# Kernel tuning notes

Measured on AMD Instinct MI355X. Metric: run time of the kernel, lower is better.

## Reference

```python
import jax, jax.numpy as jnp
import numpy as np

B, T, H, V = 32, 256, 1024, 50257


def setup_inputs() -> dict:
    key = jax.random.key(0)
    k1, k2, k3, k4 = jax.random.split(key, 4)
    # log-normalized HMM parameters, matching torch.log_softmax in __init__
    alpha = jax.nn.log_softmax(jax.random.normal(k1, (H, H), dtype=jnp.float32), axis=1)
    beta = jax.nn.log_softmax(jax.random.normal(k2, (H, V), dtype=jnp.float32), axis=1)
    gamma = jax.nn.log_softmax(jax.random.normal(k3, (H,), dtype=jnp.float32), axis=0)
    x = jax.random.randint(k4, (B, T), 0, V)
    return {"x": x, "alpha": alpha, "beta": beta, "gamma": gamma}


def reference(x, alpha, beta, gamma):
    # emission log-probs gathered per token: e[b, t, h] = beta[h, x[b, t]]
    e = beta.T[x]  # [B, T, H]

    # backward-in-time recurrence:
    #   y_{T-1} = e[:, T-1]
    #   y_t     = logsumexp_j(alpha[i, j] + y_{t+1}[b, j]) + e[:, t]
    y0 = e[:, -1]  # [B, H]

    def step(y, e_t):
        y = jax.nn.logsumexp(alpha[None, :, :] + y[:, None, :], axis=2) + e_t
        return y, None

    # scan over t = T-2 .. 0 (reverse time order)
    es = jnp.flip(e[:, :-1], axis=1).transpose(1, 0, 2)  # [T-1, B, H]
    y, _ = jax.lax.scan(step, y0, es)

    # final marginalization over initial-state distribution gamma
    return jax.nn.logsumexp(gamma[None, :] + y, axis=1)  # [B]
```

## Files before the change

kernel.cpp:

```cpp
#include <hip/hip_runtime.h>
#include <hip/hip_bf16.h>


#define Hdim 1024
#define Bdim 32
#define Tdim 256
#define Vdim 50257
#define NWG  16
#define SLICE 64

typedef __attribute__((ext_vector_type(8))) __bf16 bf16x8;
typedef __attribute__((ext_vector_type(4))) float  f32x4;
typedef __attribute__((ext_vector_type(4))) unsigned u32x4;

#define OFF_ABF   0
#define OFF_YBUF  2097152
#define OFF_PSUM  (OFF_YBUF + 131072)
#define OFF_RBUF  (OFF_PSUM + 128)
#define OFF_LREC  (OFF_RBUF + 128)
#define OFF_END0  (OFF_LREC + 8192)
#define OFF_E     (((OFF_END0) + 4095) & ~4095)
#define WS_E_NEED ((size_t)OFF_E + (size_t)Tdim * Bdim * Hdim * 4)

#define SM_A       131072
#define SM_YSH     (SM_A)
#define SM_GSH     (SM_YSH + 4096)
#define SM_LTILE   (SM_GSH + 128)
#define SMEM_BYTES (SM_LTILE + 512)

__device__ __forceinline__ void st_b128_sc(void* p, u32x4 v) {
    asm volatile("global_store_dwordx4 %0, %1, off sc0 sc1" :: "v"(p), "v"(v) : "memory");
}
__device__ __forceinline__ void st_b32_sc(void* p, unsigned v) {
    asm volatile("global_store_dword %0, %1, off sc0 sc1" :: "v"(p), "v"(v) : "memory");
}
__device__ __forceinline__ void st_f32_sc(void* p, float v) {
    asm volatile("global_store_dword %0, %1, off sc0 sc1" :: "v"(p), "v"(v) : "memory");
}
__device__ __forceinline__ u32x4 ld_b128_sc(const void* p) {
    u32x4 r;
    asm volatile("global_load_dwordx4 %0, %1, off sc0 sc1" : "=v"(r) : "v"(p) : "memory");
    return r;
}
__device__ __forceinline__ float ld_f32_sc(const void* p) {
    float r;
    asm volatile("global_load_dword %0, %1, off sc0 sc1" : "=v"(r) : "v"(p) : "memory");
    return r;
}
__device__ __forceinline__ void waitcnt_vm0() {
    asm volatile("s_waitcnt vmcnt(0)" ::: "memory");
    __builtin_amdgcn_sched_barrier(0);
}

__global__ void k_expA(const float* __restrict__ alpha, __bf16* __restrict__ Abf) {
    int idx = (blockIdx.x * 256 + threadIdx.x) * 4;
    float4 v = *(const float4*)(alpha + idx);
    union { __bf16 h[4]; uint2 u; } cv;
    cv.h[0] = (__bf16)__expf(v.x);
    cv.h[1] = (__bf16)__expf(v.y);
    cv.h[2] = (__bf16)__expf(v.z);
    cv.h[3] = (__bf16)__expf(v.w);
    *(uint2*)(Abf + idx) = cv.u;
}

__global__ void k_gather(const int* __restrict__ x, const float* __restrict__ beta,
                         float* __restrict__ E) {
    int tb = blockIdx.x;
    int t  = tb >> 5, b = tb & 31;
    int xv = x[b * Tdim + t];
    int i  = threadIdx.x * 4;
    float4 v;
    v.x = beta[(size_t)(i + 0) * Vdim + xv];
    v.y = beta[(size_t)(i + 1) * Vdim + xv];
    v.z = beta[(size_t)(i + 2) * Vdim + xv];
    v.w = beta[(size_t)(i + 3) * Vdim + xv];
    *(float4*)(E + ((size_t)t * Bdim + b) * Hdim + i) = v;
}

__device__ __forceinline__ void wait_flags(const char* lrec, int par, unsigned want) {
    if (threadIdx.x < 64) {
        const unsigned* fp =
            (const unsigned*)(lrec + ((size_t)par * NWG + (threadIdx.x & 15)) * 256 + 128);
        while (!__all((int)(__hip_atomic_load(fp, __ATOMIC_RELAXED, __HIP_MEMORY_SCOPE_AGENT) >= want)))
            __builtin_amdgcn_s_sleep(1);
    }
    __syncthreads();
}

__device__ __forceinline__ void load_e(const float* __restrict__ E,
                                       const float* __restrict__ beta,
                                       const int* __restrict__ x,
                                       int t, int b0, int i0, int useE, float e[2][4]) {
    if (useE) {
        #pragma unroll
        for (int u = 0; u < 2; ++u)
            #pragma unroll
            for (int r = 0; r < 4; ++r)
                e[u][r] = E[((size_t)t * Bdim + (b0 + r)) * Hdim + i0 + u * 16];
    } else {
        int xv[4];
        #pragma unroll
        for (int r = 0; r < 4; ++r) xv[r] = x[(b0 + r) * Tdim + t];
        #pragma unroll
        for (int u = 0; u < 2; ++u)
            #pragma unroll
            for (int r = 0; r < 4; ++r)
                e[u][r] = beta[(size_t)(i0 + u * 16) * Vdim + xv[r]];
    }
}

__device__ __forceinline__ void store_phase(const float y[2][4], const float Gc[4],
                                            char* Yblk,
                                            char* Lrec_p,
                                            __bf16* Ysh, float* Ltile,
                                            int w, int li, int g, int np, int b0,
                                            unsigned seq) {
    #pragma unroll
    for (int r = 0; r < 4; ++r) {
        #pragma unroll
        for (int u = 0; u < 2; ++u) {
            float Yn = __expf(y[u][r] - Gc[r]);
            Ysh[(b0 + r) * 64 + np * 32 + u * 16 + li] = (__bf16)Yn;
        }
        float m = fmaxf(y[0][r], y[1][r]);
        m = fmaxf(m, __shfl_xor(m, 1, 16));
        m = fmaxf(m, __shfl_xor(m, 2, 16));
        m = fmaxf(m, __shfl_xor(m, 4, 16));
        m = fmaxf(m, __shfl_xor(m, 8, 16));
        if (li == 0) Ltile[w * 32 + b0 + r] = m;
    }
    __syncthreads();
    const int tid = threadIdx.x;
    st_b128_sc(Yblk + tid * 16, ((const u32x4*)Ysh)[tid]);
    if (tid < 32) {
        int mbb = tid >> 4;
        float L = fmaxf(Ltile[mbb * 32 + tid], Ltile[(mbb + 2) * 32 + tid]);
        st_f32_sc(Lrec_p + tid * 4, L);
    }
    asm volatile("s_waitcnt vmcnt(0)" ::: "memory");
    __syncthreads();
    if (tid == 0) st_b32_sc(Lrec_p + 128, seq);
}

__launch_bounds__(256, 1)
__global__ void k_hmm(const int* __restrict__ x,
                      const float* __restrict__ beta,
                      const float* __restrict__ gamma,
                      const __bf16* __restrict__ Abf,
                      char* __restrict__ Yb,
                      char* __restrict__ lrec,
                      float* __restrict__ Psum,
                      float* __restrict__ Rbuf,
                      const float* __restrict__ Ebuf,
                      int useE)
{
    extern __shared__ char smem[];
    char*   Asl   = smem;
    __bf16* Ysh   = (__bf16*)(smem + SM_YSH);
    float*  Gsh   = (float*)(smem + SM_GSH);
    float*  Ltile = (float*)(smem + SM_LTILE);

    const int p   = blockIdx.x;
    const int tid = threadIdx.x;
    const int w   = tid >> 6;
    const int l   = tid & 63;
    const int g   = l >> 4;
    const int li  = l & 15;
    const int mb  = w & 1;
    const int np  = w >> 1;
    const int b0  = mb * 16 + g * 4;
    const int i0  = p * SLICE + np * 32 + li;

    #pragma unroll
    for (int rep = 0; rep < 32; ++rep) {
        int flat = rep * 256 + tid;
        int row  = flat >> 7;
        int c16  = flat & 127;
        uint4 v = *(const uint4*)((const char*)Abf + (size_t)(p * 64 + row) * 2048 + c16 * 16);
        int off = (row * 2048 + c16 * 16) ^ ((row & 7) << 4);
        *(uint4*)(Asl + off) = v;
    }
    __syncthreads();

    {
        float y0[2][4];
        load_e(Ebuf, beta, x, Tdim - 1, b0, i0, useE, y0);
        float Gc0[4] = {0.f, 0.f, 0.f, 0.f};
        store_phase(y0, Gc0, Yb + p * 4096, lrec + (size_t)p * 256,
                    Ysh, Ltile, w, li, g, np, b0, 1u);
    }

    float Nprev[4] = {0.f, 0.f, 0.f, 0.f};
    float ereg[2][4];
    load_e(Ebuf, beta, x, Tdim - 2, b0, i0, useE, ereg);

    for (int s = 1; s < Tdim; ++s) {
        const int t     = Tdim - 1 - s;
        const int par_r = (s - 1) & 1;
        const int par_w = s & 1;

        float eregN[2][4];
        if (s < Tdim - 1) load_e(Ebuf, beta, x, t - 1, b0, i0, useE, eregN);

        float gl[2] = {0.f, 0.f};
        if (s == Tdim - 1) { gl[0] = gamma[i0]; gl[1] = gamma[i0 + 16]; }

        wait_flags(lrec, par_r, (unsigned)s);

        const char* Ybase = Yb + (size_t)par_r * (NWG * 4096);
        const char* yrow  = Ybase + (mb * 16 + li) * 128 + g * 16;
        u32x4 yreg[32];
        #pragma unroll
        for (int kc = 0; kc < 32; ++kc)
            yreg[kc] = ld_b128_sc(yrow + (kc >> 1) * 4096 + (kc & 1) * 64);

        float gmv[16];
        const char* lbase = lrec + (size_t)par_r * NWG * 256;
        if (tid < 32) {
            #pragma unroll
            for (int q = 0; q < 16; ++q)
                gmv[q] = ld_f32_sc(lbase + q * 256 + tid * 4);
        }

        waitcnt_vm0();

        if (tid < 32) {
            float gm = gmv[0];
            #pragma unroll
            for (int q = 1; q < 16; ++q) gm = fmaxf(gm, gmv[q]);
            Gsh[tid] = gm;
        }
        __syncthreads();

        f32x4 acc0 = {0.f, 0.f, 0.f, 0.f}, acc1 = {0.f, 0.f, 0.f, 0.f};
        {
            const int ia = np * 32 + li;
            const int ib = ia + 16;
            const int basea = ia * 2048 + g * 16, xa = (ia & 7) << 4;
            const int baseb = ib * 2048 + g * 16, xb = (ib & 7) << 4;
            #pragma unroll
            for (int kc = 0; kc < 32; ++kc) {
                bf16x8 af0 = *(const bf16x8*)(Asl + ((basea + kc * 64) ^ xa));
                bf16x8 af1 = *(const bf16x8*)(Asl + ((baseb + kc * 64) ^ xb));
                bf16x8 yf  = __builtin_bit_cast(bf16x8, yreg[kc]);
                acc0 = __builtin_amdgcn_mfma_f32_16x16x32_bf16(yf, af0, acc0, 0, 0, 0);
                acc1 = __builtin_amdgcn_mfma_f32_16x16x32_bf16(yf, af1, acc1, 0, 0, 0);
            }
        }

        float Gcur[4];
        #pragma unroll
        for (int r = 0; r < 4; ++r) Gcur[r] = Gsh[b0 + r];

        float yv[2][4];
        #pragma unroll
        for (int r = 0; r < 4; ++r) {
            yv[0][r] = Nprev[r] + __logf(acc0[r]) + ereg[0][r];
            yv[1][r] = Nprev[r] + __logf(acc1[r]) + ereg[1][r];
        }

        if (s < Tdim - 1) {
            store_phase(yv, Gcur, Yb + (size_t)par_w * (NWG * 4096) + p * 4096,
                        lrec + ((size_t)par_w * NWG + p) * 256,
                        Ysh, Ltile, w, li, g, np, b0, (unsigned)(s + 1));
            #pragma unroll
            for (int r = 0; r < 4; ++r) Nprev[r] = Gcur[r];
            #pragma unroll
            for (int u = 0; u < 2; ++u)
                #pragma unroll
                for (int r = 0; r < 4; ++r) ereg[u][r] = eregN[u][r];
        } else {
            #pragma unroll
            for (int r = 0; r < 4; ++r) {
                float pa = __expf(gl[0] + yv[0][r] - Gcur[r])
                         + __expf(gl[1] + yv[1][r] - Gcur[r]);
                pa += __shfl_xor(pa, 1, 16);
                pa += __shfl_xor(pa, 2, 16);
                pa += __shfl_xor(pa, 4, 16);
                pa += __shfl_xor(pa, 8, 16);
                if (li == 0) {
                    atomicAdd(&Psum[b0 + r], pa);
                    if (p == 0) Rbuf[b0 + r] = Gcur[r];
                }
            }
        }
    }
}

__global__ void k_final(const float* __restrict__ Psum, const float* __restrict__ Rbuf,
                        float* __restrict__ out) {
    int b = threadIdx.x;
    if (b < 32) out[b] = Rbuf[b] + __logf(Psum[b]);
}

extern "C" void kernel_launch(void* const* d_in, const int* in_sizes, int n_in,
                              void* d_out, int out_size, void* d_ws, size_t ws_size,
                              hipStream_t stream) {
    const int*   x     = (const int*)d_in[0];
    const float* alpha = (const float*)d_in[1];
    const float* beta  = (const float*)d_in[2];
    const float* gamma = (const float*)d_in[3];

    char* ws = (char*)d_ws;
    __bf16* Abf  = (__bf16*)(ws + OFF_ABF);
    char*   Yb   = ws + OFF_YBUF;
    float*  Psum = (float*)(ws + OFF_PSUM);
    float*  Rbuf = (float*)(ws + OFF_RBUF);
    char*   lrec = ws + OFF_LREC;
    float*  Ebuf = (float*)(ws + OFF_E);

    int useE = (ws_size >= WS_E_NEED) ? 1 : 0;

    (void)hipMemsetAsync(ws + OFF_PSUM, 0, OFF_END0 - OFF_PSUM, stream);

    hipLaunchKernelGGL(k_expA, dim3((Hdim * Hdim) / (256 * 4)), dim3(256), 0, stream, alpha, Abf);

    if (useE)
        hipLaunchKernelGGL(k_gather, dim3(Tdim * Bdim), dim3(256), 0, stream, x, beta, Ebuf);

    (void)hipFuncSetAttribute((const void*)k_hmm, hipFuncAttributeMaxDynamicSharedMemorySize, SMEM_BYTES);
    hipLaunchKernelGGL(k_hmm, dim3(NWG), dim3(256), SMEM_BYTES, stream,
                       x, beta, gamma, Abf, Yb, lrec, Psum, Rbuf,
                       useE ? Ebuf : (const float*)nullptr, useE);

    hipLaunchKernelGGL(k_final, dim3(1), dim3(64), 0, stream, Psum, Rbuf, (float*)d_out);
}
```

Before: 2.119 ms.

## Co-locate persistent workgroups on one XCC and use cheaper cache-scope sync

The launch grows to 512 workgroups. The first workgroups found on one XCC (home chosen by CAS on the XCC id) claim the 16 compute slots and the rest exit. A runtime handshake then checks that plain sc0 stores and loads are visible across the 16 workgroups. If they are, the recurrence runs with sc0-only global accesses instead of sc0 sc1 system-scope ones, cutting the latency of each inter-workgroup exchange per timestep. The cost is extra launch overhead, a verification phase, and reliance on residency and cache-coherence behaviour, with a fallback to the old path if the check fails.

```diff
diff --git a/kernel.cpp b/kernel.cpp
--- a/kernel.cpp
+++ b/kernel.cpp
@@ -8,6 +8,8 @@
 #define Vdim 50257
 #define NWG  16
 #define SLICE 64
+#define NBLK 512
+#define VBOUND 1500
 
 typedef __attribute__((ext_vector_type(8))) __bf16 bf16x8;
 typedef __attribute__((ext_vector_type(4))) float  f32x4;
@@ -18,7 +20,9 @@
 #define OFF_PSUM  (OFF_YBUF + 131072)
 #define OFF_RBUF  (OFF_PSUM + 128)
 #define OFF_LREC  (OFF_RBUF + 128)
-#define OFF_END0  (OFF_LREC + 8192)
+#define OFF_CTL   (OFF_LREC + 8192)
+#define OFF_VER   (OFF_CTL + 128)
+#define OFF_END0  (OFF_VER + 256)
 #define OFF_E     (((OFF_END0) + 4095) & ~4095)
 #define WS_E_NEED ((size_t)OFF_E + (size_t)Tdim * Bdim * Hdim * 4)
 
@@ -28,23 +32,54 @@
 #define SM_LTILE   (SM_GSH + 128)
 #define SMEM_BYTES (SM_LTILE + 512)
 
-__device__ __forceinline__ void st_b128_sc(void* p, u32x4 v) {
-    asm volatile("global_store_dwordx4 %0, %1, off sc0 sc1" :: "v"(p), "v"(v) : "memory");
-}
-__device__ __forceinline__ void st_b32_sc(void* p, unsigned v) {
-    asm volatile("global_store_dword %0, %1, off sc0 sc1" :: "v"(p), "v"(v) : "memory");
-}
-__device__ __forceinline__ void st_f32_sc(void* p, float v) {
-    asm volatile("global_store_dword %0, %1, off sc0 sc1" :: "v"(p), "v"(v) : "memory");
-}
-__device__ __forceinline__ u32x4 ld_b128_sc(const void* p) {
+template<bool SC1>
+__device__ __forceinline__ void st_b128_x(void* p, u32x4 v) {
+    if constexpr (SC1)
+        asm volatile("global_store_dwordx4 %0, %1, off sc0 sc1" :: "v"(p), "v"(v) : "memory");
+    else
+        asm volatile("global_store_dwordx4 %0, %1, off sc0" :: "v"(p), "v"(v) : "memory");
+}
+template<bool SC1>
+__device__ __forceinline__ void st_b32_x(void* p, unsigned v) {
+    if constexpr (SC1)
+        asm volatile("global_store_dword %0, %1, off sc0 sc1" :: "v"(p), "v"(v) : "memory");
+    else
+        asm volatile("global_store_dword %0, %1, off sc0" :: "v"(p), "v"(v) : "memory");
+}
+template<bool SC1>
+__device__ __forceinline__ void st_f32_x(void* p, float v) {
+    if constexpr (SC1)
+        asm volatile("global_store_dword %0, %1, off sc0 sc1" :: "v"(p), "v"(v) : "memory");
+    else
+        asm volatile("global_store_dword %0, %1, off sc0" :: "v"(p), "v"(v) : "memory");
+}
+template<bool SC1>
+__device__ __forceinline__ u32x4 ld_b128_x(const void* p) {
     u32x4 r;
-    asm volatile("global_load_dwordx4 %0, %1, off sc0 sc1" : "=v"(r) : "v"(p) : "memory");
+    if constexpr (SC1)
+        asm volatile("global_load_dwordx4 %0, %1, off sc0 sc1" : "=v"(r) : "v"(p) : "memory");
+    else
+        asm volatile("global_load_dwordx4 %0, %1, off sc0" : "=v"(r) : "v"(p) : "memory");
     return r;
 }
-__device__ __forceinline__ float ld_f32_sc(const void* p) {
+template<bool SC1>
+__device__ __forceinline__ float ld_f32_x(const void* p) {
     float r;
-    asm volatile("global_load_dword %0, %1, off sc0 sc1" : "=v"(r) : "v"(p) : "memory");
+    if constexpr (SC1)
+        asm volatile("global_load_dword %0, %1, off sc0 sc1" : "=v"(r) : "v"(p) : "memory");
+    else
+        asm volatile("global_load_dword %0, %1, off sc0" : "=v"(r) : "v"(p) : "memory");
+    return r;
+}
+template<bool SC1>
+__device__ __forceinline__ unsigned ld_u32sync_x(const void* p) {
+    unsigned r;
+    if constexpr (SC1)
+        asm volatile("global_load_dword %0, %1, off sc0 sc1\n\ts_waitcnt vmcnt(0)"
+                     : "=v"(r) : "v"(p) : "memory");
+    else
+        asm volatile("global_load_dword %0, %1, off sc0\n\ts_waitcnt vmcnt(0)"
+                     : "=v"(r) : "v"(p) : "memory");
     return r;
 }
 __device__ __forceinline__ void waitcnt_vm0() {
@@ -77,11 +112,11 @@
     *(float4*)(E + ((size_t)t * Bdim + b) * Hdim + i) = v;
 }
 
+template<bool SC1>
 __device__ __forceinline__ void wait_flags(const char* lrec, int par, unsigned want) {
     if (threadIdx.x < 64) {
-        const unsigned* fp =
-            (const unsigned*)(lrec + ((size_t)par * NWG + (threadIdx.x & 15)) * 256 + 128);
-        while (!__all((int)(__hip_atomic_load(fp, __ATOMIC_RELAXED, __HIP_MEMORY_SCOPE_AGENT) >= want)))
+        const char* fp = lrec + ((size_t)par * NWG + (threadIdx.x & 15)) * 256 + 128;
+        while (!__all((int)(ld_u32sync_x<SC1>(fp) >= want)))
             __builtin_amdgcn_s_sleep(1);
     }
     __syncthreads();
@@ -109,11 +144,11 @@
     }
 }
 
+template<bool SC1>
 __device__ __forceinline__ void store_phase(const float y[2][4], const float Gc[4],
-                                            char* Yblk,
-                                            char* Lrec_p,
+                                            char* Yblk, char* Lrec_p,
                                             __bf16* Ysh, float* Ltile,
-                                            int w, int li, int g, int np, int b0,
+                                            int w, int li, int np, int b0,
                                             unsigned seq) {
     #pragma unroll
     for (int r = 0; r < 4; ++r) {
@@ -131,63 +166,37 @@
     }
     __syncthreads();
     const int tid = threadIdx.x;
-    st_b128_sc(Yblk + tid * 16, ((const u32x4*)Ysh)[tid]);
+    st_b128_x<SC1>(Yblk + tid * 16, ((const u32x4*)Ysh)[tid]);
     if (tid < 32) {
         int mbb = tid >> 4;
         float L = fmaxf(Ltile[mbb * 32 + tid], Ltile[(mbb + 2) * 32 + tid]);
-        st_f32_sc(Lrec_p + tid * 4, L);
+        st_f32_x<SC1>(Lrec_p + tid * 4, L);
     }
     asm volatile("s_waitcnt vmcnt(0)" ::: "memory");
     __syncthreads();
-    if (tid == 0) st_b32_sc(Lrec_p + 128, seq);
-}
-
-__launch_bounds__(256, 1)
-__global__ void k_hmm(const int* __restrict__ x,
-                      const float* __restrict__ beta,
-                      const float* __restrict__ gamma,
-                      const __bf16* __restrict__ Abf,
-                      char* __restrict__ Yb,
-                      char* __restrict__ lrec,
-                      float* __restrict__ Psum,
-                      float* __restrict__ Rbuf,
-                      const float* __restrict__ Ebuf,
-                      int useE)
-{
-    extern __shared__ char smem[];
-    char*   Asl   = smem;
-    __bf16* Ysh   = (__bf16*)(smem + SM_YSH);
-    float*  Gsh   = (float*)(smem + SM_GSH);
-    float*  Ltile = (float*)(smem + SM_LTILE);
-
-    const int p   = blockIdx.x;
+    if (tid == 0) st_b32_x<SC1>(Lrec_p + 128, seq);
+}
+
+template<bool SC1>
+__device__ __forceinline__ void hmm_body(const int* __restrict__ x,
+                                         const float* __restrict__ beta,
+                                         const float* __restrict__ gamma,
+                                         char* __restrict__ Yb,
+                                         char* __restrict__ lrec,
+                                         float* __restrict__ Psum,
+                                         float* __restrict__ Rbuf,
+                                         const float* __restrict__ Ebuf, int useE,
+                                         char* Asl, __bf16* Ysh, float* Gsh, float* Ltile,
+                                         int p, int w, int li, int g, int mb, int np,
+                                         int b0, int i0) {
     const int tid = threadIdx.x;
-    const int w   = tid >> 6;
-    const int l   = tid & 63;
-    const int g   = l >> 4;
-    const int li  = l & 15;
-    const int mb  = w & 1;
-    const int np  = w >> 1;
-    const int b0  = mb * 16 + g * 4;
-    const int i0  = p * SLICE + np * 32 + li;
-
-    #pragma unroll
-    for (int rep = 0; rep < 32; ++rep) {
-        int flat = rep * 256 + tid;
-        int row  = flat >> 7;
-        int c16  = flat & 127;
-        uint4 v = *(const uint4*)((const char*)Abf + (size_t)(p * 64 + row) * 2048 + c16 * 16);
-        int off = (row * 2048 + c16 * 16) ^ ((row & 7) << 4);
-        *(uint4*)(Asl + off) = v;
-    }
-    __syncthreads();
 
     {
         float y0[2][4];
         load_e(Ebuf, beta, x, Tdim - 1, b0, i0, useE, y0);
         float Gc0[4] = {0.f, 0.f, 0.f, 0.f};
-        store_phase(y0, Gc0, Yb + p * 4096, lrec + (size_t)p * 256,
-                    Ysh, Ltile, w, li, g, np, b0, 1u);
+        store_phase<SC1>(y0, Gc0, Yb + p * 4096, lrec + (size_t)p * 256,
+                         Ysh, Ltile, w, li, np, b0, 1u);
     }
 
     float Nprev[4] = {0.f, 0.f, 0.f, 0.f};
@@ -205,21 +214,21 @@
         float gl[2] = {0.f, 0.f};
         if (s == Tdim - 1) { gl[0] = gamma[i0]; gl[1] = gamma[i0 + 16]; }
 
-        wait_flags(lrec, par_r, (unsigned)s);
+        wait_flags<SC1>(lrec, par_r, (unsigned)s);
 
         const char* Ybase = Yb + (size_t)par_r * (NWG * 4096);
         const char* yrow  = Ybase + (mb * 16 + li) * 128 + g * 16;
         u32x4 yreg[32];
         #pragma unroll
         for (int kc = 0; kc < 32; ++kc)
-            yreg[kc] = ld_b128_sc(yrow + (kc >> 1) * 4096 + (kc & 1) * 64);
+            yreg[kc] = ld_b128_x<SC1>(yrow + (kc >> 1) * 4096 + (kc & 1) * 64);
 
         float gmv[16];
         const char* lbase = lrec + (size_t)par_r * NWG * 256;
         if (tid < 32) {
             #pragma unroll
             for (int q = 0; q < 16; ++q)
-                gmv[q] = ld_f32_sc(lbase + q * 256 + tid * 4);
+                gmv[q] = ld_f32_x<SC1>(lbase + q * 256 + tid * 4);
         }
 
         waitcnt_vm0();
@@ -260,9 +269,9 @@
         }
 
         if (s < Tdim - 1) {
-            store_phase(yv, Gcur, Yb + (size_t)par_w * (NWG * 4096) + p * 4096,
-                        lrec + ((size_t)par_w * NWG + p) * 256,
-                        Ysh, Ltile, w, li, g, np, b0, (unsigned)(s + 1));
+            store_phase<SC1>(yv, Gcur, Yb + (size_t)par_w * (NWG * 4096) + p * 4096,
+                             lrec + ((size_t)par_w * NWG + p) * 256,
+                             Ysh, Ltile, w, li, np, b0, (unsigned)(s + 1));
             #pragma unroll
             for (int r = 0; r < 4; ++r) Nprev[r] = Gcur[r];
             #pragma unroll
@@ -287,6 +296,113 @@
     }
 }
 
+__launch_bounds__(256, 1)
+__global__ void k_hmm(const int* __restrict__ x,
+                      const float* __restrict__ beta,
+                      const float* __restrict__ gamma,
+                      const __bf16* __restrict__ Abf,
+                      char* __restrict__ Yb,
+                      char* __restrict__ lrec,
+                      float* __restrict__ Psum,
+                      float* __restrict__ Rbuf,
+                      int* __restrict__ ctl,
+                      char* __restrict__ ver,
+                      const float* __restrict__ Ebuf,
+                      int useE)
+{
+    extern __shared__ char smem[];
+    char*   Asl   = smem;
+    __bf16* Ysh   = (__bf16*)(smem + SM_YSH);
+    float*  Gsh   = (float*)(smem + SM_GSH);
+    float*  Ltile = (float*)(smem + SM_LTILE);
+    __shared__ int s_slot;
+    __shared__ int s_fast;
+
+    const int tid = threadIdx.x;
+
+    if (tid == 0) {
+        unsigned xcc;
+        asm volatile("s_getreg_b32 %0, hwreg(HW_REG_XCC_ID)" : "=s"(xcc));
+        int home = atomicCAS(ctl, -1, (int)xcc);
+        if (home == -1) home = (int)xcc;
+        int slot = -1;
+        if ((int)xcc == home || blockIdx.x >= NBLK - NWG) {
+            int sl = atomicAdd(ctl + 16, 1);
+            if (sl < NWG) slot = sl;
+        }
+        s_slot = slot;
+    }
+    __syncthreads();
+    const int p = s_slot;
+    if (p < 0) return;
+
+    const int w   = tid >> 6;
+    const int l   = tid & 63;
+    const int g   = l >> 4;
+    const int li  = l & 15;
+    const int mb  = w & 1;
+    const int np  = w >> 1;
+    const int b0  = mb * 16 + g * 4;
+    const int i0  = p * SLICE + np * 32 + li;
+
+    #pragma unroll
+    for (int rep = 0; rep < 32; ++rep) {
+        int flat = rep * 256 + tid;
+        int row  = flat >> 7;
+        int c16  = flat & 127;
+        uint4 v = *(const uint4*)((const char*)Abf + (size_t)(p * 64 + row) * 2048 + c16 * 16);
+        int off = (row * 2048 + c16 * 16) ^ ((row & 7) << 4);
+        *(uint4*)(Asl + off) = v;
+    }
+    __syncthreads();
+
+    if (tid < 64) {
+        int ok = 1;
+        #pragma unroll
+        for (int round = 0; round < 2; ++round) {
+            unsigned base = round ? 0xA5000000u : 0x5A000000u;
+            if (tid == 0) {
+                st_b32_x<false>(ver + p * 4, base | (unsigned)p);
+                asm volatile("s_waitcnt vmcnt(0)" ::: "memory");
+            }
+            int seen = 1;
+            if (tid < 16) {
+                const char* tp = ver + tid * 4;
+                unsigned expect = base | (unsigned)tid;
+                seen = 0;
+                for (int it = 0; it < VBOUND; ++it) {
+                    if (ld_u32sync_x<false>(tp) == expect) { seen = 1; break; }
+                    __builtin_amdgcn_s_sleep(1);
+                }
+            }
+            ok &= __all(seen);
+        }
+        if (tid == 0) {
+            st_b32_x<true>(ver + 128 + p * 4, ok ? 1u : 2u);
+            asm volatile("s_waitcnt vmcnt(0)" ::: "memory");
+        }
+        int myfast = 1;
+        if (tid < 16) {
+            const char* vp = ver + 128 + tid * 4;
+            unsigned v;
+            while ((v = ld_u32sync_x<true>(vp)) == 0u)
+                __builtin_amdgcn_s_sleep(1);
+            myfast = (v == 1u);
+        }
+        int f = __all(myfast);
+        if (tid == 0) s_fast = f;
+    }
+    __syncthreads();
+    const int fast = s_fast;
+
+    if (fast)
+        hmm_body<false>(x, beta, gamma, Yb, lrec, Psum, Rbuf, Ebuf, useE,
+                        Asl, Ysh, Gsh, Ltile, p, w, li, g, mb, np, b0, i0);
+    else
+        hmm_body<true>(x, beta, gamma, Yb, lrec, Psum, Rbuf, Ebuf, useE,
+                       Asl, Ysh, Gsh, Ltile, p, w, li, g, mb, np, b0, i0);
+}
+
 __global__ void k_final(const float* __restrict__ Psum, const float* __restrict__ Rbuf,
                         float* __restrict__ out) {
     int b = threadIdx.x;
@@ -307,11 +423,14 @@
     float*  Psum = (float*)(ws + OFF_PSUM);
     float*  Rbuf = (float*)(ws + OFF_RBUF);
     char*   lrec = ws + OFF_LREC;
+    int*    ctl  = (int*)(ws + OFF_CTL);
+    char*   ver  = ws + OFF_VER;
     float*  Ebuf = (float*)(ws + OFF_E);
 
     int useE = (ws_size >= WS_E_NEED) ? 1 : 0;
 
     (void)hipMemsetAsync(ws + OFF_PSUM, 0, OFF_END0 - OFF_PSUM, stream);
+    (void)hipMemsetAsync(ws + OFF_CTL, 0xFF, 4, stream);
 
     hipLaunchKernelGGL(k_expA, dim3((Hdim * Hdim) / (256 * 4)), dim3(256), 0, stream, alpha, Abf);
 
@@ -319,8 +438,8 @@
         hipLaunchKernelGGL(k_gather, dim3(Tdim * Bdim), dim3(256), 0, stream, x, beta, Ebuf);
 
     (void)hipFuncSetAttribute((const void*)k_hmm, hipFuncAttributeMaxDynamicSharedMemorySize, SMEM_BYTES);
-    hipLaunchKernelGGL(k_hmm, dim3(NWG), dim3(256), SMEM_BYTES, stream,
-                       x, beta, gamma, Abf, Yb, lrec, Psum, Rbuf,
+    hipLaunchKernelGGL(k_hmm, dim3(NBLK), dim3(256), SMEM_BYTES, stream,
+                       x, beta, gamma, Abf, Yb, lrec, Psum, Rbuf, ctl, ver,
                        useE ? Ebuf : (const float*)nullptr, useE);
 
     hipLaunchKernelGGL(k_final, dim3(1), dim3(64), 0, stream, Psum, Rbuf, (float*)d_out);
```

Measured after the change: 3.617 ms. +70.7%, slower.

## Replace block-level barriers with per-wave flags and direct global publishing

Applied to the files above, without the earlier changes.

Each wave now writes its bf16 state slice and per-batch max straight to global memory and raises its own flag, so the LDS staging and __syncthreads barriers in the publish and consume phases are gone. Consumers poll 64 per-wave flags with one lane each and compute the global max via shuffles instead of shared memory. The max loads are overlapped with the MFMA loop through a partial vmcnt wait. In exchange there are many small 16-bit system-coherent stores and more flag traffic per step.

```diff
diff --git a/kernel.cpp b/kernel.cpp
--- a/kernel.cpp
+++ b/kernel.cpp
@@ -17,16 +17,14 @@
 #define OFF_YBUF  2097152
 #define OFF_PSUM  (OFF_YBUF + 131072)
 #define OFF_RBUF  (OFF_PSUM + 128)
-#define OFF_LREC  (OFF_RBUF + 128)
-#define OFF_END0  (OFF_LREC + 8192)
+#define OFF_WREC  (OFF_RBUF + 128)
+#define OFF_FLG   (OFF_WREC + 8192)
+#define OFF_END0  (OFF_FLG + 8192)
 #define OFF_E     (((OFF_END0) + 4095) & ~4095)
 #define WS_E_NEED ((size_t)OFF_E + (size_t)Tdim * Bdim * Hdim * 4)
 
 #define SM_A       131072
-#define SM_YSH     (SM_A)
-#define SM_GSH     (SM_YSH + 4096)
-#define SM_LTILE   (SM_GSH + 128)
-#define SMEM_BYTES (SM_LTILE + 512)
+#define SMEM_BYTES (SM_A + 256)
 
 __device__ __forceinline__ void st_b128_sc(void* p, u32x4 v) {
     asm volatile("global_store_dwordx4 %0, %1, off sc0 sc1" :: "v"(p), "v"(v) : "memory");
@@ -34,8 +32,8 @@
 __device__ __forceinline__ void st_b32_sc(void* p, unsigned v) {
     asm volatile("global_store_dword %0, %1, off sc0 sc1" :: "v"(p), "v"(v) : "memory");
 }
-__device__ __forceinline__ void st_f32_sc(void* p, float v) {
-    asm volatile("global_store_dword %0, %1, off sc0 sc1" :: "v"(p), "v"(v) : "memory");
+__device__ __forceinline__ void st_b16_sc(void* p, unsigned v) {
+    asm volatile("global_store_short %0, %1, off sc0 sc1" :: "v"(p), "v"(v) : "memory");
 }
 __device__ __forceinline__ u32x4 ld_b128_sc(const void* p) {
     u32x4 r;
@@ -47,8 +45,18 @@
     asm volatile("global_load_dword %0, %1, off sc0 sc1" : "=v"(r) : "v"(p) : "memory");
     return r;
 }
+__device__ __forceinline__ unsigned ld_u32sync_sc(const void* p) {
+    unsigned r;
+    asm volatile("global_load_dword %0, %1, off sc0 sc1\n\ts_waitcnt vmcnt(0)"
+                 : "=v"(r) : "v"(p) : "memory");
+    return r;
+}
 __device__ __forceinline__ void waitcnt_vm0() {
     asm volatile("s_waitcnt vmcnt(0)" ::: "memory");
+    __builtin_amdgcn_sched_barrier(0);
+}
+__device__ __forceinline__ void waitcnt_vm32() {
+    asm volatile("s_waitcnt vmcnt(32)" ::: "memory");
     __builtin_amdgcn_sched_barrier(0);
 }
 
@@ -77,16 +85,6 @@
     *(float4*)(E + ((size_t)t * Bdim + b) * Hdim + i) = v;
 }
 
-__device__ __forceinline__ void wait_flags(const char* lrec, int par, unsigned want) {
-    if (threadIdx.x < 64) {
-        const unsigned* fp =
-            (const unsigned*)(lrec + ((size_t)par * NWG + (threadIdx.x & 15)) * 256 + 128);
-        while (!__all((int)(__hip_atomic_load(fp, __ATOMIC_RELAXED, __HIP_MEMORY_SCOPE_AGENT) >= want)))
-            __builtin_amdgcn_s_sleep(1);
-    }
-    __syncthreads();
-}
-
 __device__ __forceinline__ void load_e(const float* __restrict__ E,
                                        const float* __restrict__ beta,
                                        const int* __restrict__ x,
@@ -109,37 +107,35 @@
     }
 }
 
-__device__ __forceinline__ void store_phase(const float y[2][4], const float Gc[4],
-                                            char* Yblk,
-                                            char* Lrec_p,
-                                            __bf16* Ysh, float* Ltile,
-                                            int w, int li, int g, int np, int b0,
-                                            unsigned seq) {
+__device__ __forceinline__ void publish_wave(const float y[2][4], const float Gc[4],
+                                             char* Yblk,
+                                             char* wrec_pw,
+                                             char* flg_pw,
+                                             int li, int g, int np, int b0,
+                                             unsigned seq) {
+    float mx[4];
     #pragma unroll
     for (int r = 0; r < 4; ++r) {
         #pragma unroll
         for (int u = 0; u < 2; ++u) {
             float Yn = __expf(y[u][r] - Gc[r]);
-            Ysh[(b0 + r) * 64 + np * 32 + u * 16 + li] = (__bf16)Yn;
+            __bf16 h = (__bf16)Yn;
+            unsigned hv = (unsigned)__builtin_bit_cast(unsigned short, h);
+            st_b16_sc(Yblk + (b0 + r) * 128 + (np * 32 + u * 16 + li) * 2, hv);
         }
         float m = fmaxf(y[0][r], y[1][r]);
         m = fmaxf(m, __shfl_xor(m, 1, 16));
         m = fmaxf(m, __shfl_xor(m, 2, 16));
         m = fmaxf(m, __shfl_xor(m, 4, 16));
         m = fmaxf(m, __shfl_xor(m, 8, 16));
-        if (li == 0) Ltile[w * 32 + b0 + r] = m;
-    }
-    __syncthreads();
-    const int tid = threadIdx.x;
-    st_b128_sc(Yblk + tid * 16, ((const u32x4*)Ysh)[tid]);
-    if (tid < 32) {
-        int mbb = tid >> 4;
-        float L = fmaxf(Ltile[mbb * 32 + tid], Ltile[(mbb + 2) * 32 + tid]);
-        st_f32_sc(Lrec_p + tid * 4, L);
+        mx[r] = m;
+    }
+    if (li == 0) {
+        f32x4 mv = {mx[0], mx[1], mx[2], mx[3]};
+        st_b128_sc(wrec_pw + g * 16, __builtin_bit_cast(u32x4, mv));
     }
     asm volatile("s_waitcnt vmcnt(0)" ::: "memory");
-    __syncthreads();
-    if (tid == 0) st_b32_sc(Lrec_p + 128, seq);
+    if ((threadIdx.x & 63) == 0) st_b32_sc(flg_pw, seq);
 }
 
 __launch_bounds__(256, 1)
@@ -148,17 +144,15 @@
                       const float* __restrict__ gamma,
                       const __bf16* __restrict__ Abf,
                       char* __restrict__ Yb,
-                      char* __restrict__ lrec,
+                      char* __restrict__ wrec,
+                      char* __restrict__ flg,
                       float* __restrict__ Psum,
                       float* __restrict__ Rbuf,
                       const float* __restrict__ Ebuf,
                       int useE)
 {
     extern __shared__ char smem[];
-    char*   Asl   = smem;
-    __bf16* Ysh   = (__bf16*)(smem + SM_YSH);
-    float*  Gsh   = (float*)(smem + SM_GSH);
-    float*  Ltile = (float*)(smem + SM_LTILE);
+    char* Asl = smem;
 
     const int p   = blockIdx.x;
     const int tid = threadIdx.x;
@@ -186,8 +180,10 @@
         float y0[2][4];
         load_e(Ebuf, beta, x, Tdim - 1, b0, i0, useE, y0);
         float Gc0[4] = {0.f, 0.f, 0.f, 0.f};
-        store_phase(y0, Gc0, Yb + p * 4096, lrec + (size_t)p * 256,
-                    Ysh, Ltile, w, li, g, np, b0, 1u);
+        publish_wave(y0, Gc0, Yb + p * 4096,
+                     wrec + (size_t)p * 256 + w * 64,
+                     flg + (size_t)(p * 4 + w) * 64,
+                     li, g, np, b0, 1u);
     }
 
     float Nprev[4] = {0.f, 0.f, 0.f, 0.f};
@@ -201,11 +197,14 @@
 
         float eregN[2][4];
         if (s < Tdim - 1) load_e(Ebuf, beta, x, t - 1, b0, i0, useE, eregN);
-
         float gl[2] = {0.f, 0.f};
         if (s == Tdim - 1) { gl[0] = gamma[i0]; gl[1] = gamma[i0 + 16]; }
-
-        wait_flags(lrec, par_r, (unsigned)s);
+        waitcnt_vm0();
+
+        {
+            const char* fp = flg + (size_t)par_r * 4096 + l * 64;
+            while (!__all((int)(ld_u32sync_sc(fp) >= (unsigned)s))) {}
+        }
 
         const char* Ybase = Yb + (size_t)par_r * (NWG * 4096);
         const char* yrow  = Ybase + (mb * 16 + li) * 128 + g * 16;
@@ -214,23 +213,21 @@
         for (int kc = 0; kc < 32; ++kc)
             yreg[kc] = ld_b128_sc(yrow + (kc >> 1) * 4096 + (kc & 1) * 64);
 
-        float gmv[16];
-        const char* lbase = lrec + (size_t)par_r * NWG * 256;
-        if (tid < 32) {
-            #pragma unroll
-            for (int q = 0; q < 16; ++q)
-                gmv[q] = ld_f32_sc(lbase + q * 256 + tid * 4);
-        }
-
-        waitcnt_vm0();
-
-        if (tid < 32) {
-            float gm = gmv[0];
-            #pragma unroll
-            for (int q = 1; q < 16; ++q) gm = fmaxf(gm, gmv[q]);
-            Gsh[tid] = gm;
-        }
-        __syncthreads();
+        float gmv[32];
+        {
+            const char* wbase = wrec + (size_t)par_r * 4096;
+            if (l < 32) {
+                int bmb = l >> 4;
+                int idx = (l & 15) * 4;
+                #pragma unroll
+                for (int q = 0; q < 16; ++q) {
+                    gmv[2 * q]     = ld_f32_sc(wbase + q * 256 + bmb * 64 + idx);
+                    gmv[2 * q + 1] = ld_f32_sc(wbase + q * 256 + (bmb + 2) * 64 + idx);
+                }
+            }
+        }
+
+        waitcnt_vm32();
 
         f32x4 acc0 = {0.f, 0.f, 0.f, 0.f}, acc1 = {0.f, 0.f, 0.f, 0.f};
         {
@@ -248,9 +245,16 @@
             }
         }
 
+        waitcnt_vm0();
+
+        float gm = -3.0e38f;
+        if (l < 32) {
+            #pragma unroll
+            for (int q = 0; q < 32; ++q) gm = fmaxf(gm, gmv[q]);
+        }
         float Gcur[4];
         #pragma unroll
-        for (int r = 0; r < 4; ++r) Gcur[r] = Gsh[b0 + r];
+        for (int r = 0; r < 4; ++r) Gcur[r] = __shfl(gm, b0 + r);
 
         float yv[2][4];
         #pragma unroll
@@ -260,9 +264,11 @@
         }
 
         if (s < Tdim - 1) {
-            store_phase(yv, Gcur, Yb + (size_t)par_w * (NWG * 4096) + p * 4096,
-                        lrec + ((size_t)par_w * NWG + p) * 256,
-                        Ysh, Ltile, w, li, g, np, b0, (unsigned)(s + 1));
+            publish_wave(yv, Gcur,
+                         Yb + (size_t)par_w * (NWG * 4096) + p * 4096,
+                         wrec + (size_t)par_w * 4096 + (size_t)p * 256 + w * 64,
+                         flg + (size_t)par_w * 4096 + (size_t)(p * 4 + w) * 64,
+                         li, g, np, b0, (unsigned)(s + 1));
             #pragma unroll
             for (int r = 0; r < 4; ++r) Nprev[r] = Gcur[r];
             #pragma unroll
@@ -306,7 +312,8 @@
     char*   Yb   = ws + OFF_YBUF;
     float*  Psum = (float*)(ws + OFF_PSUM);
     float*  Rbuf = (float*)(ws + OFF_RBUF);
-    char*   lrec = ws + OFF_LREC;
+    char*   wrec = ws + OFF_WREC;
+    char*   flg  = ws + OFF_FLG;
     float*  Ebuf = (float*)(ws + OFF_E);
 
     int useE = (ws_size >= WS_E_NEED) ? 1 : 0;
@@ -320,7 +327,7 @@
 
     (void)hipFuncSetAttribute((const void*)k_hmm, hipFuncAttributeMaxDynamicSharedMemorySize, SMEM_BYTES);
     hipLaunchKernelGGL(k_hmm, dim3(NWG), dim3(256), SMEM_BYTES, stream,
-                       x, beta, gamma, Abf, Yb, lrec, Psum, Rbuf,
+                       x, beta, gamma, Abf, Yb, wrec, flg, Psum, Rbuf,
                        useE ? Ebuf : (const float*)nullptr, useE);
 
     hipLaunchKernelGGL(k_final, dim3(1), dim3(64), 0, stream, Psum, Rbuf, (float*)d_out);
```

Measured after the change: 2.018 ms. 4.8% less time.
